# Performance work log

Measured on AMD Instinct MI355X. Metric: run time of the kernel, lower is better.

The kernel has to match this reference:

```python
import jax, jax.numpy as jnp
import numpy as np

MASK_FILL = -1e9
LN_EPS = 1e-5


def setup_inputs() -> dict:
    key = jax.random.key(0)
    ks = jax.random.split(key, 8)
    b, n, d = 4, 4096, 768
    k, ds = 64, 32
    x = jax.random.normal(ks[0], (b, n, d), dtype=jnp.float32)
    encoded_descriptions = jax.random.normal(ks[1], (k, ds, d), dtype=jnp.float32)
    description_attention_mask = jax.random.randint(ks[2], (k, ds), 0, 2).astype(jnp.int32)
    attention_masks = jax.random.randint(ks[3], (b, n), 0, 2).astype(jnp.int32)
    std = 0.03
    Wk = std * jax.random.normal(ks[4], (d, d), dtype=jnp.float32)
    Wv = std * jax.random.normal(ks[5], (d, d), dtype=jnp.float32)
    Wo = std * jax.random.normal(ks[6], (1, d), dtype=jnp.float32)
    bo = jnp.zeros((1,), dtype=jnp.float32)
    ln_gamma = jnp.ones((d,), dtype=jnp.float32)
    ln_beta = jnp.zeros((d,), dtype=jnp.float32)
    return {
        "x": x,
        "encoded_descriptions": encoded_descriptions,
        "description_attention_mask": description_attention_mask,
        "attention_masks": attention_masks,
        "Wk": Wk, "Wv": Wv, "Wo": Wo, "bo": bo,
        "ln_gamma": ln_gamma, "ln_beta": ln_beta,
    }


def reference(x, encoded_descriptions, description_attention_mask, attention_masks,
              Wk, Wv, Wo, bo, ln_gamma, ln_beta):
    # x: [b, n, d]; encoded_descriptions: [k, ds, d]
    d = x.shape[-1]
    scale = 1.0 / jnp.sqrt(jnp.float32(d))

    k_note = jnp.einsum('bni,oi->bno', x, Wk)  # nn.Linear: x @ W.T
    v_note = jnp.einsum('bni,oi->bno', x, Wv)

    # att: [b, k, ds, n]  (torch computes kdbn then permutes to bkdn)
    att = jnp.einsum('kdi,bni->bkdn', encoded_descriptions, k_note) * scale

    desc_mask = description_attention_mask.astype(bool)          # [k, ds]
    note_mask = attention_masks.astype(bool)                     # [b, n]
    combined = desc_mask[None, :, :, None] & note_mask[:, None, None, :]  # [b,k,ds,n]

    att = jnp.where(combined, att, MASK_FILL)
    attention = jax.nn.softmax(att, axis=-1)                     # [b,k,ds,n]

    context = jnp.einsum('bkdn,bni->bkdi', attention, v_note)    # [b,k,ds,d]

    desc_importance = attention.sum(axis=-1)                     # [b,k,ds]
    desc_importance = jnp.where(desc_mask[None, :, :], desc_importance, MASK_FILL)
    desc_weights = jax.nn.softmax(desc_importance, axis=-1)      # [b,k,ds]

    pooled = (context * desc_weights[..., None]).sum(axis=2)     # [b,k,d]

    mu = pooled.mean(axis=-1, keepdims=True)
    var = pooled.var(axis=-1, keepdims=True)
    y = (pooled - mu) * jax.lax.rsqrt(var + LN_EPS) * ln_gamma + ln_beta

    out = jnp.einsum('bkd,od->bko', y, Wo) + bo                  # [b,k,1]
    return out[..., 0]                                           # [b,k]
```

## Files before the change

kernel.cpp:

```cpp
#include <hip/hip_runtime.h>
#include <hip/hip_bf16.h>
#include <hip/hip_fp16.h>

typedef _Float16 half8 __attribute__((ext_vector_type(8)));
typedef _Float16 half4 __attribute__((ext_vector_type(4)));
typedef _Float16 half2v __attribute__((ext_vector_type(2)));
typedef float f32x4 __attribute__((ext_vector_type(4)));

#define LN_EPS 1e-5f
#define MASK_FILL -1e9f

__device__ __forceinline__ void async16(void* lds, const void* g) {
  __builtin_amdgcn_global_load_lds(
      (__attribute__((address_space(1))) void*)(g),
      (__attribute__((address_space(3))) void*)(lds), 16, 0, 0);
}

__global__ __launch_bounds__(256) void prep_all_kernel(
    const int* __restrict__ dmask, const int* __restrict__ amask,
    int* __restrict__ rowmap, float* __restrict__ row_w,
    int* __restrict__ start, int* __restrict__ keepM,
    int* __restrict__ perm, int* __restrict__ cntN) {
  __shared__ int lsum[256];
  __shared__ int nvs[64];
  const int tid = threadIdx.x;
  if (blockIdx.x == 0) {
    int flags[8];
    int cnt = 0;
#pragma unroll
    for (int u = 0; u < 8; u++) {
      flags[u] = dmask[tid * 8 + u] != 0;
      cnt += flags[u];
    }
    if (tid < 64) {
      int c = 0;
      for (int u = 0; u < 32; u++) c += (dmask[tid * 32 + u] != 0);
      nvs[tid] = c;
    }
    lsum[tid] = cnt;
    __syncthreads();
    for (int ofs = 1; ofs < 256; ofs <<= 1) {
      int t = (tid >= ofs) ? lsum[tid - ofs] : 0;
      __syncthreads();
      lsum[tid] += t;
      __syncthreads();
    }
    int excl = lsum[tid] - cnt;
    int pos = excl;
#pragma unroll
    for (int u = 0; u < 8; u++) {
      if (flags[u]) {
        int row = tid * 8 + u;
        rowmap[pos] = row;
        row_w[pos] = 1.0f / (float)nvs[row >> 5];
        pos++;
      }
    }
    if ((tid & 3) == 0) start[tid >> 2] = excl;
    if (tid == 255) {
      start[64] = lsum[255];
      *keepM = lsum[255];
    }
  } else {
    const int b = blockIdx.x - 1;
    const int* am = amask + (size_t)b * 4096;
    int flags[16];
    int cnt = 0;
#pragma unroll
    for (int u = 0; u < 16; u++) {
      flags[u] = am[tid * 16 + u] != 0;
      cnt += flags[u];
    }
    lsum[tid] = cnt;
    __syncthreads();
    for (int ofs = 1; ofs < 256; ofs <<= 1) {
      int t = (tid >= ofs) ? lsum[tid - ofs] : 0;
      __syncthreads();
      lsum[tid] += t;
      __syncthreads();
    }
    const int total = lsum[255];
    int vpos = lsum[tid] - cnt;
    int ipos = total + (tid * 16 - vpos);
    int* pm = perm + (size_t)b * 4096;
#pragma unroll
    for (int u = 0; u < 16; u++) {
      int g = tid * 16 + u;
      if (flags[u]) pm[vpos++] = g;
      else pm[ipos++] = g;
    }
    if (tid == 0) cntN[b] = total;
  }
}

__global__ __launch_bounds__(256) void gather_cast_all_kernel(
    const float* __restrict__ x, const float* __restrict__ enc,
    const float* __restrict__ Wv, const float* __restrict__ Wk,
    const int* __restrict__ perm, const int* __restrict__ rowmap,
    const int* __restrict__ keepM,
    _Float16* __restrict__ xh_c, _Float16* __restrict__ enc_c,
    _Float16* __restrict__ wvh, _Float16* __restrict__ wkT) {
  __shared__ float tile[32][33];
  const int bid = blockIdx.x;
  const int t = threadIdx.x;
  if (bid < 16384) {
    const int b = bid >> 12, ci = bid & 4095;
    const int n = perm[(size_t)b * 4096 + ci];
    const float* s = x + ((size_t)b * 4096 + n) * 768;
    _Float16* d = xh_c + ((size_t)b * 4096 + ci) * 768;
#pragma unroll
    for (int u = 0; u < 3; u++) d[t + u * 256] = (_Float16)s[t + u * 256];
  } else if (bid < 18432) {
    const int r = bid - 16384;
    _Float16* d = enc_c + (size_t)r * 768;
    if (r < *keepM) {
      const float* s = enc + (size_t)rowmap[r] * 768;
#pragma unroll
      for (int u = 0; u < 3; u++) d[t + u * 256] = (_Float16)s[t + u * 256];
    } else {
      int* di = (int*)d;
      for (int i = t; i < 384; i += 256) di[i] = 0;
    }
  } else if (bid < 19008) {
    const int base = (bid - 18432) * 1024 + t * 4;
    float4 v = *(const float4*)(Wv + base);
    half4 h = { (_Float16)v.x, (_Float16)v.y, (_Float16)v.z, (_Float16)v.w };
    *(half4*)(wvh + base) = h;
  } else {
    const int tb = bid - 19008;
    const int bc = (tb % 24) * 32, br = (tb / 24) * 32;
    const int lc = t & 31, lr0 = t >> 5;
    for (int i = lr0; i < 32; i += 8)
      tile[i][lc] = Wk[(size_t)(br + i) * 768 + bc + lc];
    __syncthreads();
    for (int i = lr0; i < 32; i += 8)
      wkT[(size_t)(bc + i) * 768 + br + lc] = (_Float16)tile[lc][i];
  }
}

template<bool OUT_F32, bool XCD>
__global__ __launch_bounds__(256) void gemm_f16_kernel(
    const _Float16* __restrict__ A, const _Float16* __restrict__ Bt,
    void* __restrict__ C, int M, int N, int K, float alpha,
    size_t strideBt, size_t strideC, const int* __restrict__ keepRows,
    const int* __restrict__ keepN) {
  int bx = blockIdx.x, by = blockIdx.y, bz = blockIdx.z;
  if (XCD) {
    const int gx = gridDim.x, gy = gridDim.y;
    const int total = gx * gy * gridDim.z;
    const int L = bx + gx * (by + gy * bz);
    const int orig = (L & 7) * (total >> 3) + (L >> 3);
    bx = orig % gx;
    const int rest = orig / gx;
    by = rest % gy;
    bz = rest / gy;
  }
  const int bm = bx * 64, bn = by * 128;
  if (keepRows && bm >= *keepRows) return;
  if (keepN && bn >= keepN[bz]) return;
  __shared__ _Float16 As[64 * 64];
  __shared__ _Float16 Bs[128 * 64];
  const int tid = threadIdx.x;
  const size_t z = bz;
  const int wave = tid >> 6, lane = tid & 63;
  const int wr = (wave >> 1) * 32, wc = (wave & 1) * 64;
  const int fr = lane & 15, xr = lane & 7;
  f32x4 acc[2][4] = {};
  const int lrow = lane >> 3;
  const int scol = (((lane & 7) ^ lrow)) * 8;
  const _Float16* ga = A + (size_t)(bm + wave * 16 + lrow) * K + scol;
  const _Float16* gb = Bt + z * strideBt + (size_t)(bn + wave * 32 + lrow) * K + scol;
  _Float16* lA = &As[(wave * 16) * 64];
  _Float16* lB = &Bs[(wave * 32) * 64];
  for (int k0 = 0; k0 < K; k0 += 64) {
    __syncthreads();
#pragma unroll
    for (int i = 0; i < 2; i++)
      async16(lA + i * 8 * 64, ga + (size_t)(8 * i) * K + k0);
#pragma unroll
    for (int i = 0; i < 4; i++)
      async16(lB + i * 8 * 64, gb + (size_t)(8 * i) * K + k0);
    __syncthreads();
#pragma unroll
    for (int k2 = 0; k2 < 2; k2++) {
      const int sb = k2 * 4 + (lane >> 4);
      const int so = (sb ^ xr) * 8;
      half8 af[2], bf[4];
#pragma unroll
      for (int i = 0; i < 2; i++)
        af[i] = *(const half8*)&As[(wr + i * 16 + fr) * 64 + so];
#pragma unroll
      for (int j = 0; j < 4; j++)
        bf[j] = *(const half8*)&Bs[(wc + j * 16 + fr) * 64 + so];
#pragma unroll
      for (int i = 0; i < 2; i++)
#pragma unroll
        for (int j = 0; j < 4; j++)
          acc[i][j] = __builtin_amdgcn_mfma_f32_16x16x32_f16(af[i], bf[j], acc[i][j], 0, 0, 0);
    }
  }
  const int rg = (lane >> 4) * 4;
#pragma unroll
  for (int i = 0; i < 2; i++) {
#pragma unroll
    for (int j = 0; j < 4; j++) {
      int col = bn + wc + j * 16 + fr;
#pragma unroll
      for (int r = 0; r < 4; r++) {
        int row = bm + wr + i * 16 + rg + r;
        float v = acc[i][j][r] * alpha;
        if (OUT_F32)
          ((float*)C)[z * strideC + (size_t)row * N + col] = v;
        else
          ((_Float16*)C)[z * strideC + (size_t)row * N + col] = (_Float16)v;
      }
    }
  }
}

__device__ __forceinline__ float block_reduce(float v, bool do_max, float* wbuf, int tid) {
#pragma unroll
  for (int m = 32; m; m >>= 1) {
    float o = __shfl_xor(v, m);
    v = do_max ? fmaxf(v, o) : (v + o);
  }
  if ((tid & 63) == 0) wbuf[tid >> 6] = v;
  __syncthreads();
  float r = do_max ? fmaxf(fmaxf(wbuf[0], wbuf[1]), fmaxf(wbuf[2], wbuf[3]))
                   : (wbuf[0] + wbuf[1] + wbuf[2] + wbuf[3]);
  __syncthreads();
  return r;
}

__global__ __launch_bounds__(256) void row_stats_kernel(
    const _Float16* __restrict__ S, const float* __restrict__ row_w,
    const int* __restrict__ keepM, const int* __restrict__ cntN,
    float4* __restrict__ stats_c) {
  const int r = blockIdx.x;
  if (r >= *keepM) return;
  __shared__ float wbuf[4];
  const int b = blockIdx.z;
  const int tid = threadIdx.x;
  const int cnt = cntN[b];
  if (cnt == 0) return;
  const float w = row_w[r];
  const _Float16* sp = S + ((size_t)b * 2048 + r) * 4096 + tid * 16;
  float a[16];
  {
    half8 v0 = *(const half8*)(sp);
    half8 v1 = *(const half8*)(sp + 8);
    const int c0 = tid * 16;
#pragma unroll
    for (int u = 0; u < 8; u++) {
      a[u] = (c0 + u < cnt) ? (float)v0[u] : MASK_FILL;
      a[8 + u] = (c0 + 8 + u < cnt) ? (float)v1[u] : MASK_FILL;
    }
  }
  float mx = a[0];
#pragma unroll
  for (int c = 1; c < 16; c++) mx = fmaxf(mx, a[c]);
  mx = block_reduce(mx, true, wbuf, tid);
  float ls = 0.f;
#pragma unroll
  for (int c = 0; c < 16; c++) ls += expf(a[c] - mx);
  float denom = block_reduce(ls, false, wbuf, tid);
  if (tid == 0)
    stats_c[(size_t)b * 2048 + r] = make_float4(mx, w / denom, 0.f, 0.f);
}

__global__ __launch_bounds__(256) void combine_kernel(
    const _Float16* __restrict__ S, const float4* __restrict__ stats_c,
    const int* __restrict__ start, const int* __restrict__ cntN,
    float* __restrict__ ca) {
  const int kd = blockIdx.x;
  const int b = blockIdx.z;
  const int i = blockIdx.y * 512 + threadIdx.x * 2;
  const int i0 = start[kd], i1 = start[kd + 1];
  const int cnt = cntN[b];
  float acc0, acc1;
  if (i0 == i1 || cnt == 0) {
    acc0 = acc1 = 1.0f / 4096.0f;
  } else if (i >= cnt) {
    acc0 = acc1 = 0.f;
  } else {
    acc0 = 0.f;
    acc1 = 0.f;
    const _Float16* sp = S + ((size_t)b * 2048 + i0) * 4096 + i;
    for (int r = i0; r < i1; r++, sp += 4096) {
      float4 s4 = stats_c[(size_t)b * 2048 + r];
      half2v v = *(const half2v*)sp;
      acc0 += s4.y * expf((float)v[0] - s4.x);
      acc1 += s4.y * expf((float)v[1] - s4.x);
    }
    if (i + 1 >= cnt) acc1 = 0.f;
  }
  float2 rr = {acc0, acc1};
  *(float2*)&ca[((size_t)b * 64 + kd) * 4096 + i] = rr;
}

__global__ __launch_bounds__(256) void t_partial_kernel(
    const float* __restrict__ ca,
    const _Float16* __restrict__ xh,
    float* __restrict__ t_part) {
  __shared__ float cas[64][68];
  __shared__ float xs[64][132];
  const int jt = blockIdx.x;
  const int nc = blockIdx.y;
  const int b = blockIdx.z;
  const int tid = threadIdx.x;
  const int tm = tid >> 4, tj = tid & 15;
  const int r = tid >> 2;
  const int cg = (tid & 3) * 16;
  const int cc = (tid & 3) * 32;
  float acc[4][8] = {};
  for (int n0 = nc * 256; n0 < nc * 256 + 256; n0 += 64) {
    __syncthreads();
    const float* cap = ca + (size_t)(b * 64 + r) * 4096 + n0 + cg;
#pragma unroll
    for (int u = 0; u < 16; u += 4)
      *(float4*)&cas[r][cg + u] = *(const float4*)(cap + u);
    const _Float16* xp = xh + ((size_t)b * 4096 + n0 + r) * 768 + jt * 128 + cc;
#pragma unroll
    for (int u = 0; u < 32; u += 8) {
      half8 hv = *(const half8*)(xp + u);
#pragma unroll
      for (int q = 0; q < 8; q++) xs[r][cc + u + q] = (float)hv[q];
    }
    __syncthreads();
#pragma unroll 8
    for (int nn = 0; nn < 64; ++nn) {
      float cm[4], xj[8];
#pragma unroll
      for (int i = 0; i < 4; i++) cm[i] = cas[tm * 4 + i][nn];
#pragma unroll
      for (int j = 0; j < 8; j++) xj[j] = xs[nn][tj * 8 + j];
#pragma unroll
      for (int i = 0; i < 4; i++)
#pragma unroll
        for (int j = 0; j < 8; j++) acc[i][j] += cm[i] * xj[j];
    }
  }
#pragma unroll
  for (int i = 0; i < 4; i++)
#pragma unroll
    for (int j = 0; j < 8; j++)
      t_part[((size_t)nc * 256 + b * 64 + tm * 4 + i) * 768 + jt * 128 + tj * 8 + j] = acc[i][j];
}

__global__ __launch_bounds__(256) void t_reduce_kernel(
    const float* __restrict__ t_part, _Float16* __restrict__ th) {
  int i = blockIdx.x * 256 + threadIdx.x;
  float s = 0.f;
#pragma unroll
  for (int nc = 0; nc < 16; ++nc) s += t_part[(size_t)nc * 196608 + i];
  th[i] = (_Float16)s;
}

__global__ __launch_bounds__(256) void ln_out_kernel(
    const float* __restrict__ pooled, const float* __restrict__ Wo,
    const float* __restrict__ bo, const float* __restrict__ gamma,
    const float* __restrict__ beta, float* __restrict__ out) {
  __shared__ float wbuf[4];
  const int row = blockIdx.x, tid = threadIdx.x;
  float p[3];
#pragma unroll
  for (int u = 0; u < 3; u++) p[u] = pooled[(size_t)row * 768 + tid + u * 256];
  float s1 = p[0] + p[1] + p[2];
  float s2 = p[0] * p[0] + p[1] * p[1] + p[2] * p[2];
  s1 = block_reduce(s1, false, wbuf, tid);
  s2 = block_reduce(s2, false, wbuf, tid);
  float mean = s1 * (1.f / 768.f);
  float var = s2 * (1.f / 768.f) - mean * mean;
  float rstd = rsqrtf(var + LN_EPS);
  float accv = 0.f;
#pragma unroll
  for (int u = 0; u < 3; u++) {
    int i = tid + u * 256;
    float y = (p[u] - mean) * rstd * gamma[i] + beta[i];
    accv += y * Wo[i];
  }
  accv = block_reduce(accv, false, wbuf, tid);
  if (tid == 0) out[row] = accv + bo[0];
}

extern "C" void kernel_launch(void* const* d_in, const int* in_sizes, int n_in,
                              void* d_out, int out_size, void* d_ws, size_t ws_size,
                              hipStream_t stream) {
  const float* x = (const float*)d_in[0];
  const float* enc = (const float*)d_in[1];
  const int* dmask = (const int*)d_in[2];
  const int* amask = (const int*)d_in[3];
  const float* Wk = (const float*)d_in[4];
  const float* Wv = (const float*)d_in[5];
  const float* Wo = (const float*)d_in[6];
  const float* bo = (const float*)d_in[7];
  const float* gamma = (const float*)d_in[8];
  const float* beta = (const float*)d_in[9];
  float* out = (float*)d_out;

  char* ws = (char*)d_ws;
  size_t off = 0;
  auto alloc = [&](size_t bytes) -> char* {
    char* p = ws + off;
    off += (bytes + 255) & ~((size_t)255);
    return p;
  };
  _Float16* xh_c = (_Float16*)alloc((size_t)16384 * 768 * 2);
  _Float16* wkT = (_Float16*)alloc((size_t)768 * 768 * 2);
  _Float16* wvh = (_Float16*)alloc((size_t)768 * 768 * 2);
  _Float16* enc_c = (_Float16*)alloc((size_t)2048 * 768 * 2);
  _Float16* encK_c = (_Float16*)alloc((size_t)2048 * 768 * 2);
  float* ca = (float*)alloc((size_t)4 * 64 * 4096 * 4);
  float* t_part = (float*)alloc((size_t)16 * 256 * 768 * 4);
  _Float16* th = (_Float16*)alloc((size_t)256 * 768 * 2);
  float* pooled = (float*)alloc((size_t)256 * 768 * 4);
  float4* stats_c = (float4*)alloc((size_t)4 * 2048 * 16);
  int* rowmap = (int*)alloc(2048 * 4);
  float* row_w = (float*)alloc(2048 * 4);
  int* start = (int*)alloc(65 * 4);
  int* keepM = (int*)alloc(4);
  int* perm = (int*)alloc((size_t)4 * 4096 * 4);
  int* cntN = (int*)alloc(4 * 4);

  const size_t s_one = (size_t)2048 * 4096 * 2;
  const bool batched = (off + 4 * s_one) <= ws_size;
  _Float16* S = (_Float16*)alloc(batched ? 4 * s_one : s_one);

  const float scale = 0.036084391824351615f;

  prep_all_kernel<<<5, 256, 0, stream>>>(
      dmask, amask, rowmap, row_w, start, keepM, perm, cntN);
  gather_cast_all_kernel<<<19584, 256, 0, stream>>>(
      x, enc, Wv, Wk, perm, rowmap, keepM, xh_c, enc_c, wvh, wkT);

  gemm_f16_kernel<false, false><<<dim3(32, 6), 256, 0, stream>>>(
      enc_c, wkT, encK_c, 2048, 768, 768, 1.0f, 0, 0, keepM, nullptr);

  if (batched) {
    gemm_f16_kernel<false, true><<<dim3(32, 32, 4), 256, 0, stream>>>(
        encK_c, xh_c, S, 2048, 4096, 768, scale,
        (size_t)4096 * 768, (size_t)2048 * 4096, keepM, cntN);
    row_stats_kernel<<<dim3(2048, 1, 4), 256, 0, stream>>>(
        S, row_w, keepM, cntN, stats_c);
    combine_kernel<<<dim3(64, 8, 4), 256, 0, stream>>>(
        S, stats_c, start, cntN, ca);
  } else {
    for (int b = 0; b < 4; b++) {
      gemm_f16_kernel<false, true><<<dim3(32, 32), 256, 0, stream>>>(
          encK_c, xh_c + (size_t)b * 4096 * 768, S, 2048, 4096, 768, scale,
          0, 0, keepM, cntN + b);
      row_stats_kernel<<<dim3(2048, 1, 1), 256, 0, stream>>>(
          S, row_w, keepM, cntN + b, stats_c + (size_t)b * 2048);
      combine_kernel<<<dim3(64, 8, 1), 256, 0, stream>>>(
          S, stats_c + (size_t)b * 2048, start, cntN + b,
          ca + (size_t)b * 64 * 4096);
    }
  }

  t_partial_kernel<<<dim3(6, 16, 4), 256, 0, stream>>>(ca, xh_c, t_part);
  t_reduce_kernel<<<768, 256, 0, stream>>>(t_part, th);
  gemm_f16_kernel<true, false><<<dim3(4, 6), 256, 0, stream>>>(
      th, wvh, pooled, 256, 768, 768, 1.0f, 0, 0, nullptr, nullptr);
  ln_out_kernel<<<256, 256, 0, stream>>>(pooled, Wo, bo, gamma, beta, out);
}
```

Baseline: 141.4 us.

## Fuse softmax row statistics into score GEMM epilogue, drop row_stats kernel

The score GEMM epilogue now computes, for each 64-column slice, a per-row max and sum of exponentials from the fp32 accumulators and writes them as partials. The combine kernel merges these partials per row into a max and inverse-weighted denominator held in shared memory. This removes the separate row_stats kernel, which made a full extra read pass over the large fp16 score matrix. In exchange the GEMM epilogue does extra exp and shuffle work. The statistics now come from fp32 values rather than fp16-rounded ones, which is a small numeric difference.

```diff
diff --git a/kernel.cpp b/kernel.cpp
--- a/kernel.cpp
+++ b/kernel.cpp
@@ -138,12 +138,12 @@
   }
 }
 
-template<bool OUT_F32, bool XCD>
+template<bool OUT_F32, bool XCD, bool STATS>
 __global__ __launch_bounds__(256) void gemm_f16_kernel(
     const _Float16* __restrict__ A, const _Float16* __restrict__ Bt,
     void* __restrict__ C, int M, int N, int K, float alpha,
     size_t strideBt, size_t strideC, const int* __restrict__ keepRows,
-    const int* __restrict__ keepN) {
+    const int* __restrict__ keepN, float2* __restrict__ partials) {
   int bx = blockIdx.x, by = blockIdx.y, bz = blockIdx.z;
   if (XCD) {
     const int gx = gridDim.x, gy = gridDim.y;
@@ -216,6 +216,60 @@
       }
     }
   }
+  if (STATS) {
+    const int cnt = keepN[bz];
+    float m[2][4];
+#pragma unroll
+    for (int i = 0; i < 2; i++)
+#pragma unroll
+      for (int r = 0; r < 4; r++) m[i][r] = MASK_FILL;
+#pragma unroll
+    for (int i = 0; i < 2; i++)
+#pragma unroll
+      for (int j = 0; j < 4; j++) {
+        const bool valid = (bn + wc + j * 16 + fr) < cnt;
+#pragma unroll
+        for (int r = 0; r < 4; r++) {
+          float v = valid ? acc[i][j][r] * alpha : MASK_FILL;
+          m[i][r] = fmaxf(m[i][r], v);
+        }
+      }
+#pragma unroll
+    for (int mask = 1; mask < 16; mask <<= 1)
+#pragma unroll
+      for (int i = 0; i < 2; i++)
+#pragma unroll
+        for (int r = 0; r < 4; r++)
+          m[i][r] = fmaxf(m[i][r], __shfl_xor(m[i][r], mask));
+    float ps[2][4] = {};
+#pragma unroll
+    for (int i = 0; i < 2; i++)
+#pragma unroll
+      for (int j = 0; j < 4; j++) {
+        const bool valid = (bn + wc + j * 16 + fr) < cnt;
+#pragma unroll
+        for (int r = 0; r < 4; r++)
+          ps[i][r] += valid ? expf(acc[i][j][r] * alpha - m[i][r]) : 0.f;
+      }
+#pragma unroll
+    for (int mask = 1; mask < 16; mask <<= 1)
+#pragma unroll
+      for (int i = 0; i < 2; i++)
+#pragma unroll
+        for (int r = 0; r < 4; r++)
+          ps[i][r] += __shfl_xor(ps[i][r], mask);
+    if ((lane & 15) == 0) {
+      const int g = lane >> 4;
+      const int cb = (bn + wc) >> 6;
+#pragma unroll
+      for (int i = 0; i < 2; i++)
+#pragma unroll
+        for (int r = 0; r < 4; r++) {
+          int row = bm + wr + i * 16 + g * 4 + r;
+          partials[((size_t)bz * 2048 + row) * 32 + cb] = make_float2(m[i][r], ps[i][r]);
+        }
+    }
+  }
 }
 
 __device__ __forceinline__ float block_reduce(float v, bool do_max, float* wbuf, int tid) {
@@ -232,67 +286,48 @@
   return r;
 }
 
-__global__ __launch_bounds__(256) void row_stats_kernel(
-    const _Float16* __restrict__ S, const float* __restrict__ row_w,
-    const int* __restrict__ keepM, const int* __restrict__ cntN,
-    float4* __restrict__ stats_c) {
-  const int r = blockIdx.x;
-  if (r >= *keepM) return;
-  __shared__ float wbuf[4];
+__global__ __launch_bounds__(256) void combine_kernel(
+    const _Float16* __restrict__ S, const float2* __restrict__ partials,
+    const float* __restrict__ row_w, const int* __restrict__ start,
+    const int* __restrict__ cntN, float* __restrict__ ca) {
+  __shared__ float smx[32], siw[32];
+  const int kd = blockIdx.x;
   const int b = blockIdx.z;
   const int tid = threadIdx.x;
-  const int cnt = cntN[b];
-  if (cnt == 0) return;
-  const float w = row_w[r];
-  const _Float16* sp = S + ((size_t)b * 2048 + r) * 4096 + tid * 16;
-  float a[16];
-  {
-    half8 v0 = *(const half8*)(sp);
-    half8 v1 = *(const half8*)(sp + 8);
-    const int c0 = tid * 16;
-#pragma unroll
-    for (int u = 0; u < 8; u++) {
-      a[u] = (c0 + u < cnt) ? (float)v0[u] : MASK_FILL;
-      a[8 + u] = (c0 + 8 + u < cnt) ? (float)v1[u] : MASK_FILL;
-    }
-  }
-  float mx = a[0];
-#pragma unroll
-  for (int c = 1; c < 16; c++) mx = fmaxf(mx, a[c]);
-  mx = block_reduce(mx, true, wbuf, tid);
-  float ls = 0.f;
-#pragma unroll
-  for (int c = 0; c < 16; c++) ls += expf(a[c] - mx);
-  float denom = block_reduce(ls, false, wbuf, tid);
-  if (tid == 0)
-    stats_c[(size_t)b * 2048 + r] = make_float4(mx, w / denom, 0.f, 0.f);
-}
-
-__global__ __launch_bounds__(256) void combine_kernel(
-    const _Float16* __restrict__ S, const float4* __restrict__ stats_c,
-    const int* __restrict__ start, const int* __restrict__ cntN,
-    float* __restrict__ ca) {
-  const int kd = blockIdx.x;
-  const int b = blockIdx.z;
-  const int i = blockIdx.y * 512 + threadIdx.x * 2;
+  const int i = blockIdx.y * 512 + tid * 2;
   const int i0 = start[kd], i1 = start[kd + 1];
   const int cnt = cntN[b];
   float acc0, acc1;
   if (i0 == i1 || cnt == 0) {
     acc0 = acc1 = 1.0f / 4096.0f;
-  } else if (i >= cnt) {
-    acc0 = acc1 = 0.f;
   } else {
-    acc0 = 0.f;
-    acc1 = 0.f;
-    const _Float16* sp = S + ((size_t)b * 2048 + i0) * 4096 + i;
-    for (int r = i0; r < i1; r++, sp += 4096) {
-      float4 s4 = stats_c[(size_t)b * 2048 + r];
-      half2v v = *(const half2v*)sp;
-      acc0 += s4.y * expf((float)v[0] - s4.x);
-      acc1 += s4.y * expf((float)v[1] - s4.x);
-    }
-    if (i + 1 >= cnt) acc1 = 0.f;
+    const int nr = i1 - i0;
+    if (tid < nr) {
+      const int r = i0 + tid;
+      const float2* pp = partials + ((size_t)b * 2048 + r) * 32;
+      const int nb = (cnt + 63) >> 6;
+      float mx = MASK_FILL;
+      for (int k = 0; k < nb; k++) mx = fmaxf(mx, pp[k].x);
+      float denom = 0.f;
+      for (int k = 0; k < nb; k++) denom += pp[k].y * expf(pp[k].x - mx);
+      smx[tid] = mx;
+      siw[tid] = row_w[r] / denom;
+    }
+    __syncthreads();
+    if (i >= cnt) {
+      acc0 = acc1 = 0.f;
+    } else {
+      acc0 = 0.f;
+      acc1 = 0.f;
+      const _Float16* sp = S + ((size_t)b * 2048 + i0) * 4096 + i;
+      for (int r = 0; r < nr; r++, sp += 4096) {
+        const float mx = smx[r], iw = siw[r];
+        half2v v = *(const half2v*)sp;
+        acc0 += iw * expf((float)v[0] - mx);
+        acc1 += iw * expf((float)v[1] - mx);
+      }
+      if (i + 1 >= cnt) acc1 = 0.f;
+    }
   }
   float2 rr = {acc0, acc1};
   *(float2*)&ca[((size_t)b * 64 + kd) * 4096 + i] = rr;
@@ -414,7 +449,7 @@
   float* t_part = (float*)alloc((size_t)16 * 256 * 768 * 4);
   _Float16* th = (_Float16*)alloc((size_t)256 * 768 * 2);
   float* pooled = (float*)alloc((size_t)256 * 768 * 4);
-  float4* stats_c = (float4*)alloc((size_t)4 * 2048 * 16);
+  float2* partials = (float2*)alloc((size_t)4 * 2048 * 32 * 8);
   int* rowmap = (int*)alloc(2048 * 4);
   float* row_w = (float*)alloc(2048 * 4);
   int* start = (int*)alloc(65 * 4);
@@ -433,33 +468,28 @@
   gather_cast_all_kernel<<<19584, 256, 0, stream>>>(
       x, enc, Wv, Wk, perm, rowmap, keepM, xh_c, enc_c, wvh, wkT);
 
-  gemm_f16_kernel<false, false><<<dim3(32, 6), 256, 0, stream>>>(
-      enc_c, wkT, encK_c, 2048, 768, 768, 1.0f, 0, 0, keepM, nullptr);
+  gemm_f16_kernel<false, false, false><<<dim3(32, 6), 256, 0, stream>>>(
+      enc_c, wkT, encK_c, 2048, 768, 768, 1.0f, 0, 0, keepM, nullptr, nullptr);
 
   if (batched) {
-    gemm_f16_kernel<false, true><<<dim3(32, 32, 4), 256, 0, stream>>>(
+    gemm_f16_kernel<false, true, true><<<dim3(32, 32, 4), 256, 0, stream>>>(
         encK_c, xh_c, S, 2048, 4096, 768, scale,
-        (size_t)4096 * 768, (size_t)2048 * 4096, keepM, cntN);
-    row_stats_kernel<<<dim3(2048, 1, 4), 256, 0, stream>>>(
-        S, row_w, keepM, cntN, stats_c);
+        (size_t)4096 * 768, (size_t)2048 * 4096, keepM, cntN, partials);
     combine_kernel<<<dim3(64, 8, 4), 256, 0, stream>>>(
-        S, stats_c, start, cntN, ca);
+        S, partials, row_w, start, cntN, ca);
   } else {
     for (int b = 0; b < 4; b++) {
-      gemm_f16_kernel<false, true><<<dim3(32, 32), 256, 0, stream>>>(
+      gemm_f16_kernel<false, true, true><<<dim3(32, 32), 256, 0, stream>>>(
           encK_c, xh_c + (size_t)b * 4096 * 768, S, 2048, 4096, 768, scale,
-          0, 0, keepM, cntN + b);
-      row_stats_kernel<<<dim3(2048, 1, 1), 256, 0, stream>>>(
-          S, row_w, keepM, cntN + b, stats_c + (size_t)b * 2048);
+          0, 0, keepM, cntN + b, partials);
       combine_kernel<<<dim3(64, 8, 1), 256, 0, stream>>>(
-          S, stats_c + (size_t)b * 2048, start, cntN + b,
-          ca + (size_t)b * 64 * 4096);
+          S, partials, row_w, start, cntN + b, ca + (size_t)b * 64 * 4096);
     }
   }
 
   t_partial_kernel<<<dim3(6, 16, 4), 256, 0, stream>>>(ca, xh_c, t_part);
   t_reduce_kernel<<<768, 256, 0, stream>>>(t_part, th);
-  gemm_f16_kernel<true, false><<<dim3(4, 6), 256, 0, stream>>>(
-      th, wvh, pooled, 256, 768, 768, 1.0f, 0, 0, nullptr, nullptr);
+  gemm_f16_kernel<true, false, false><<<dim3(4, 6), 256, 0, stream>>>(
+      th, wvh, pooled, 256, 768, 768, 1.0f, 0, 0, nullptr, nullptr, nullptr);
   ln_out_kernel<<<256, 256, 0, stream>>>(pooled, Wo, bo, gamma, beta, out);
 }
```

Result: slower. 145.5 us (+2.9%).
